# Kernel tuning notes

Hardware: AMD Instinct MI355X
Metric: run time of the kernel (lower is better)

Reference implementation:

```python
import jax, jax.numpy as jnp
from jax import lax
import numpy as np

BATCH, SEQ, VOCAB, EMB, UNIT = 256, 512, 50000, 128, 512


def setup_inputs() -> dict:
    key = jax.random.key(0)
    ks = jax.random.split(key, 8)
    s = 0.05  # keep tanh out of saturation
    return {
        "tokens": jax.random.randint(ks[0], (BATCH, SEQ), 0, VOCAB, dtype=jnp.int32),
        "emb": jax.random.normal(ks[1], (VOCAB, EMB), jnp.float32) * s,
        "Wx0": jax.random.normal(ks[2], (EMB, UNIT), jnp.float32) * s,
        "Wh0": jax.random.normal(ks[3], (UNIT, UNIT), jnp.float32) * s,
        "b0": jnp.zeros((UNIT,), jnp.float32),
        "Wx1": jax.random.normal(ks[4], (UNIT, UNIT), jnp.float32) * s,
        "Wh1": jax.random.normal(ks[5], (UNIT, UNIT), jnp.float32) * s,
        "b1": jnp.zeros((UNIT,), jnp.float32),
        "fc_w": jax.random.normal(ks[6], (UNIT, 1), jnp.float32) * s,
        "fc_b": jnp.zeros((1,), jnp.float32),
    }


def reference(tokens, emb, Wx0, Wh0, b0, Wx1, Wh1, b1, fc_w, fc_b):
    # Embedding lookup: [B, T, E]
    x = emb[tokens]
    B = tokens.shape[0]
    U = Wh0.shape[0]

    def step(carry, xt):
        h0, h1, h2 = carry
        # SimpleRNNCell: h' = tanh(x @ Wx + h @ Wh + b); dropout inactive (training=None)
        h0n = jnp.tanh(xt @ Wx0 + h0 @ Wh0 + b0)
        # NOTE: original code reuses rnncell1 weights for both layer 1 and layer 2 (bug kept)
        h1n = jnp.tanh(h0n @ Wx1 + h1 @ Wh1 + b1)
        h2n = jnp.tanh(h1n @ Wx1 + h2 @ Wh1 + b1)
        return (h0n, h1n, h2n), None

    init = tuple(jnp.zeros((B, U), x.dtype) for _ in range(3))
    (h0, h1, h2), _ = lax.scan(step, init, jnp.swapaxes(x, 0, 1))  # scan over time [T, B, E]
    logits = h2 @ fc_w + fc_b  # [B, 1]
    return jax.nn.sigmoid(logits)
```

## Files before the change

### kernel.cpp

```cpp
#include <hip/hip_runtime.h>


#define BATCH 256
#define SEQ   512
#define EMBD  128
#define UNIT  512

typedef _Float16 half8 __attribute__((ext_vector_type(8)));
typedef _Float16 half4 __attribute__((ext_vector_type(4)));
typedef float    f32x4 __attribute__((ext_vector_type(4)));
typedef unsigned int uint4v __attribute__((ext_vector_type(4)));
typedef int      int4v __attribute__((ext_vector_type(4)));

#define FLAGS_BYTES 4096
#define HBUF_OFF    4096
#define HBUF_ELEMS  (3*8*4*32*512)
#define HBUF_BYTES  (HBUF_ELEMS*2)
#define PWX0_OFF    (HBUF_OFF + HBUF_BYTES)
#define PWH0_OFF    (PWX0_OFF + EMBD*UNIT*2)
#define PWX1_OFF    (PWH0_OFF + UNIT*UNIT*2)
#define PWH1_OFF    (PWX1_OFF + UNIT*UNIT*2)

__device__ __forceinline__ void sc_st_int(int* p, int v) {
    asm volatile("global_store_dword %0, %1, off sc0 sc1" :: "v"(p), "v"(v) : "memory");
}

__device__ __forceinline__ void sc_ld_q3(const int* p0, const int* p1, const int* p2,
                                         int4v& a, int4v& b, int4v& c) {
    asm volatile(
        "global_load_dwordx4 %0, %3, off sc0 sc1\n\t"
        "global_load_dwordx4 %1, %4, off sc0 sc1\n\t"
        "global_load_dwordx4 %2, %5, off sc0 sc1\n\t"
        "s_waitcnt vmcnt(0)"
        : "=&v"(a), "=&v"(b), "=&v"(c)
        : "v"(p0), "v"(p1), "v"(p2)
        : "memory");
}

__device__ __forceinline__ void sc_load14(
    const uint4v* a0, const uint4v* a1, const uint4v* a2,
    const uint4v* a3, const uint4v* a4, const uint4v* a5,
    const uint4v* b0, const uint4v* b1, const uint4v* b2, const uint4v* b3,
    const uint4v* b4, const uint4v* b5, const uint4v* b6, const uint4v* b7,
    uint4v& s0, uint4v& s1, uint4v& s2, uint4v& s3, uint4v& s4, uint4v& s5,
    uint4v& r0, uint4v& r1, uint4v& r2, uint4v& r3,
    uint4v& r4, uint4v& r5, uint4v& r6, uint4v& r7)
{
    asm volatile(
        "global_load_dwordx4 %0, %14, off sc0 sc1\n\t"
        "global_load_dwordx4 %1, %15, off sc0 sc1\n\t"
        "global_load_dwordx4 %2, %16, off sc0 sc1\n\t"
        "global_load_dwordx4 %3, %17, off sc0 sc1\n\t"
        "global_load_dwordx4 %4, %18, off sc0 sc1\n\t"
        "global_load_dwordx4 %5, %19, off sc0 sc1\n\t"
        "global_load_dwordx4 %6, %20, off sc0 sc1\n\t"
        "global_load_dwordx4 %7, %21, off sc0 sc1\n\t"
        "global_load_dwordx4 %8, %22, off sc0 sc1\n\t"
        "global_load_dwordx4 %9, %23, off sc0 sc1\n\t"
        "global_load_dwordx4 %10, %24, off sc0 sc1\n\t"
        "global_load_dwordx4 %11, %25, off sc0 sc1\n\t"
        "global_load_dwordx4 %12, %26, off sc0 sc1\n\t"
        "global_load_dwordx4 %13, %27, off sc0 sc1\n\t"
        "s_waitcnt vmcnt(0)"
        : "=&v"(s0), "=&v"(s1), "=&v"(s2), "=&v"(s3), "=&v"(s4), "=&v"(s5),
          "=&v"(r0), "=&v"(r1), "=&v"(r2), "=&v"(r3),
          "=&v"(r4), "=&v"(r5), "=&v"(r6), "=&v"(r7)
        : "v"(a0), "v"(a1), "v"(a2), "v"(a3), "v"(a4), "v"(a5),
          "v"(b0), "v"(b1), "v"(b2), "v"(b3), "v"(b4), "v"(b5), "v"(b6), "v"(b7)
        : "memory");
}

__device__ __forceinline__ void sc_load6(
    const uint4v* p0, const uint4v* p1, const uint4v* p2,
    const uint4v* p3, const uint4v* p4, const uint4v* p5,
    uint4v& r0, uint4v& r1, uint4v& r2, uint4v& r3, uint4v& r4, uint4v& r5)
{
    asm volatile(
        "global_load_dwordx4 %0, %6, off sc0 sc1\n\t"
        "global_load_dwordx4 %1, %7, off sc0 sc1\n\t"
        "global_load_dwordx4 %2, %8, off sc0 sc1\n\t"
        "global_load_dwordx4 %3, %9, off sc0 sc1\n\t"
        "global_load_dwordx4 %4, %10, off sc0 sc1\n\t"
        "global_load_dwordx4 %5, %11, off sc0 sc1\n\t"
        "s_waitcnt vmcnt(0)"
        : "=&v"(r0), "=&v"(r1), "=&v"(r2), "=&v"(r3), "=&v"(r4), "=&v"(r5)
        : "v"(p0), "v"(p1), "v"(p2), "v"(p3), "v"(p4), "v"(p5)
        : "memory");
}

__device__ __forceinline__ void sc_store2(uint4v* p0, uint4v v0, uint4v* p1, uint4v v1) {
    asm volatile(
        "global_store_dwordx4 %0, %2, off sc0 sc1\n\t"
        "global_store_dwordx4 %1, %3, off sc0 sc1\n\t"
        "s_waitcnt vmcnt(0)"
        :: "v"(p0), "v"(p1), "v"(v0), "v"(v1)
        : "memory");
}

__global__ void zero_ws_kernel(uint4v* __restrict__ p, int n16) {
    int i = blockIdx.x * 256 + threadIdx.x;
    uint4v z = {0u, 0u, 0u, 0u};
    if (i < n16) p[i] = z;
}

__global__ void pack_w_kernel(const float* __restrict__ src, _Float16* __restrict__ dst,
                              int K, int N) {
    int idx = blockIdx.x * 256 + threadIdx.x;
    if (idx >= K * N) return;
    int j    = idx & 7;
    int lane = (idx >> 3) & 63;
    int rest = idx >> 9;
    int KT   = K >> 5;
    int kt   = rest % KT;
    int nt   = rest / KT;
    int k = kt*32 + (lane >> 4)*8 + j;
    int n = nt*16 + (lane & 15);
    dst[idx] = (_Float16)src[k * N + n];
}

__global__ __launch_bounds__(256, 1)
void rnn_main_kernel(const int*   __restrict__ tokens,
                     const float* __restrict__ emb,
                     const float* __restrict__ b0,
                     const float* __restrict__ b1,
                     char* ws)
{
    const int bid   = blockIdx.x;
    const int layer = bid >> 5;
    const int mg    = (bid >> 2) & 7;
    const int ns    = bid & 3;
    const int tid   = threadIdx.x;
    const int wv    = tid >> 6;
    const int lane  = tid & 63;
    const int q     = lane >> 4;
    const int c16   = lane & 15;

    int* flags = (int*)ws;
    int* qOwn  = flags + (layer*8 + mg)*32;
    int* qUp   = flags + ((layer > 0 ? layer-1 : layer)*8 + mg)*32;
    int* qDn   = flags + ((layer < 2 ? layer+1 : layer)*8 + mg)*32;

    _Float16* hbuf = (_Float16*)(ws + HBUF_OFF);
    const _Float16* pWh = (const _Float16*)(ws + (layer == 0 ? PWH0_OFF : PWH1_OFF));
    const _Float16* pWx = (const _Float16*)(ws + (layer == 0 ? PWX0_OFF : PWX1_OFF));
    const float* bias = (layer == 0) ? b0 : b1;

    const int c0  = ns*128 + wv*32;
    const int nt0 = c0 >> 4;

    __shared__ _Float16 Ah [32][512];
    __shared__ _Float16 Ain[32][512];
    __shared__ _Float16 Bounce[32][128];

    {
        uint4v z = {0u,0u,0u,0u};
#pragma unroll
        for (int i = 0; i < 8; ++i) ((uint4v*)Ah)[i*256 + tid] = z;
    }

    half8 whf[16][2];
    half8 wxf[16][2];
#pragma unroll
    for (int kt = 0; kt < 16; ++kt)
#pragma unroll
        for (int n = 0; n < 2; ++n)
            whf[kt][n] = *(const half8*)&pWh[(((nt0 + n)*16 + kt)*64 + lane) * 8];
    if (layer == 0) {
#pragma unroll
        for (int kt = 0; kt < 4; ++kt)
#pragma unroll
            for (int n = 0; n < 2; ++n)
                wxf[kt][n] = *(const half8*)&pWx[(((nt0 + n)*4 + kt)*64 + lane) * 8];
    } else {
#pragma unroll
        for (int kt = 0; kt < 16; ++kt)
#pragma unroll
            for (int n = 0; n < 2; ++n)
                wxf[kt][n] = *(const half8*)&pWx[(((nt0 + n)*16 + kt)*64 + lane) * 8];
    }

    const float bv0 = bias[c0 + c16];
    const float bv1 = bias[c0 + 16 + c16];

    const int m0       = mg * 32;
    const int slotBase = (layer*8 + mg) * 4;

    const int sA = (ns == 0) ? 1 : 0;
    const int sB = (ns <= 1) ? 2 : 1;
    const int sC = (ns <= 2) ? 3 : 2;

    for (int t = 0; t < SEQ; ++t) {
        if (tid == 0) {
            for (;;) {
                int4v o, u, d;
                sc_ld_q3(qOwn, qUp, qDn, o, u, d);
                int mo = o[0] < o[1] ? o[0] : o[1];
                mo = mo < o[2] ? mo : o[2]; mo = mo < o[3] ? mo : o[3];
                int mu = u[0] < u[1] ? u[0] : u[1];
                mu = mu < u[2] ? mu : u[2]; mu = mu < u[3] ? mu : u[3];
                int md = d[0] < d[1] ? d[0] : d[1];
                md = md < d[2] ? md : d[2]; md = md < d[3] ? md : d[3];
                bool ok = (mo >= t);
                if (layer > 0)            ok = ok && (mu >= t + 1);
                if (layer < 2 && t >= 4)  ok = ok && (md >= t - 3);
                if (ok) break;
                __builtin_amdgcn_s_sleep(1);
            }
        }
        __syncthreads();

        const uint4v* tp = (const uint4v*)(hbuf + (slotBase + ((t + 3) & 3)) * 16384);
        const int j0 = 2*tid, j1 = j0 + 1;
        const int r0i = j0 >> 4, cl0 = j0 & 15;
        const int r1i = j1 >> 4, cl1 = j1 & 15;
        const int ccA0 = sA*16 + cl0, ccA1 = sA*16 + cl1;
        const int ccB0 = sB*16 + cl0, ccB1 = sB*16 + cl1;
        const int ccC0 = sC*16 + cl0, ccC1 = sC*16 + cl1;

        f32x4 acc00 = {0,0,0,0}, acc01 = {0,0,0,0}, acc10 = {0,0,0,0}, acc11 = {0,0,0,0};

        if (layer > 0) {
            const uint4v* sb = (const uint4v*)
                (hbuf + (((layer-1)*8 + mg)*4 + (t & 3)) * 16384);
            uint4v s0,s1,s2,s3,s4,s5, rr0,rr1,rr2,rr3,rr4,rr5,rr6,rr7;
            sc_load14(tp + r0i*64 + ccA0, tp + r1i*64 + ccA1,
                      tp + r0i*64 + ccB0, tp + r1i*64 + ccB1,
                      tp + r0i*64 + ccC0, tp + r1i*64 + ccC1,
                      sb +        tid, sb +  256 + tid, sb +  512 + tid, sb +  768 + tid,
                      sb + 1024 + tid, sb + 1280 + tid, sb + 1536 + tid, sb + 1792 + tid,
                      s0, s1, s2, s3, s4, s5,
                      rr0, rr1, rr2, rr3, rr4, rr5, rr6, rr7);
            *(uint4v*)&Ah[r0i][((ccA0 + r0i) & 63) * 8] = s0;
            *(uint4v*)&Ah[r1i][((ccA1 + r1i) & 63) * 8] = s1;
            *(uint4v*)&Ah[r0i][((ccB0 + r0i) & 63) * 8] = s2;
            *(uint4v*)&Ah[r1i][((ccB1 + r1i) & 63) * 8] = s3;
            *(uint4v*)&Ah[r0i][((ccC0 + r0i) & 63) * 8] = s4;
            *(uint4v*)&Ah[r1i][((ccC1 + r1i) & 63) * 8] = s5;
#pragma unroll
            for (int i = 0; i < 8; ++i) {
                uint4v v = (i==0)?rr0:(i==1)?rr1:(i==2)?rr2:(i==3)?rr3:
                           (i==4)?rr4:(i==5)?rr5:(i==6)?rr6:rr7;
                int ci = i*256 + tid;
                int r  = ci >> 6;
                int cc = ci & 63;
                *(uint4v*)&Ain[r][((cc + r) & 63) * 8] = v;
            }
            __syncthreads();

#pragma unroll
            for (int kt = 0; kt < 16; ++kt) {
                half8 a0 = *(const half8*)&Ah[c16]     [((kt*4 + q + c16)      & 63) * 8];
                half8 a1 = *(const half8*)&Ah[16 + c16][((kt*4 + q + 16 + c16) & 63) * 8];
                acc00 = __builtin_amdgcn_mfma_f32_16x16x32_f16(a0, whf[kt][0], acc00, 0, 0, 0);
                acc01 = __builtin_amdgcn_mfma_f32_16x16x32_f16(a0, whf[kt][1], acc01, 0, 0, 0);
                acc10 = __builtin_amdgcn_mfma_f32_16x16x32_f16(a1, whf[kt][0], acc10, 0, 0, 0);
                acc11 = __builtin_amdgcn_mfma_f32_16x16x32_f16(a1, whf[kt][1], acc11, 0, 0, 0);
            }
#pragma unroll
            for (int kt = 0; kt < 16; ++kt) {
                half8 a0 = *(const half8*)&Ain[c16]     [((kt*4 + q + c16)      & 63) * 8];
                half8 a1 = *(const half8*)&Ain[16 + c16][((kt*4 + q + 16 + c16) & 63) * 8];
                acc00 = __builtin_amdgcn_mfma_f32_16x16x32_f16(a0, wxf[kt][0], acc00, 0, 0, 0);
                acc01 = __builtin_amdgcn_mfma_f32_16x16x32_f16(a0, wxf[kt][1], acc01, 0, 0, 0);
                acc10 = __builtin_amdgcn_mfma_f32_16x16x32_f16(a1, wxf[kt][0], acc10, 0, 0, 0);
                acc11 = __builtin_amdgcn_mfma_f32_16x16x32_f16(a1, wxf[kt][1], acc11, 0, 0, 0);
            }
        } else {
            uint4v s0, s1, s2, s3, s4, s5;
            sc_load6(tp + r0i*64 + ccA0, tp + r1i*64 + ccA1,
                     tp + r0i*64 + ccB0, tp + r1i*64 + ccB1,
                     tp + r0i*64 + ccC0, tp + r1i*64 + ccC1,
                     s0, s1, s2, s3, s4, s5);
            *(uint4v*)&Ah[r0i][((ccA0 + r0i) & 63) * 8] = s0;
            *(uint4v*)&Ah[r1i][((ccA1 + r1i) & 63) * 8] = s1;
            *(uint4v*)&Ah[r0i][((ccB0 + r0i) & 63) * 8] = s2;
            *(uint4v*)&Ah[r1i][((ccB1 + r1i) & 63) * 8] = s3;
            *(uint4v*)&Ah[r0i][((ccC0 + r0i) & 63) * 8] = s4;
            *(uint4v*)&Ah[r1i][((ccC1 + r1i) & 63) * 8] = s5;
#pragma unroll
            for (int i = 0; i < 4; ++i) {
                int idx = i*256 + tid;
                int r   = idx >> 5;
                int qq  = idx & 31;
                int tok = tokens[(m0 + r)*SEQ + t];
                float4 f = *((const float4*)(emb + (long)tok * EMBD) + qq);
                half4 h = { (_Float16)f.x, (_Float16)f.y, (_Float16)f.z, (_Float16)f.w };
                *(half4*)&Ain[r][((((qq >> 1) + r) & 63) * 8) + (qq & 1) * 4] = h;
            }
            __syncthreads();

#pragma unroll
            for (int kt = 0; kt < 16; ++kt) {
                half8 a0 = *(const half8*)&Ah[c16]     [((kt*4 + q + c16)      & 63) * 8];
                half8 a1 = *(const half8*)&Ah[16 + c16][((kt*4 + q + 16 + c16) & 63) * 8];
                acc00 = __builtin_amdgcn_mfma_f32_16x16x32_f16(a0, whf[kt][0], acc00, 0, 0, 0);
                acc01 = __builtin_amdgcn_mfma_f32_16x16x32_f16(a0, whf[kt][1], acc01, 0, 0, 0);
                acc10 = __builtin_amdgcn_mfma_f32_16x16x32_f16(a1, whf[kt][0], acc10, 0, 0, 0);
                acc11 = __builtin_amdgcn_mfma_f32_16x16x32_f16(a1, whf[kt][1], acc11, 0, 0, 0);
            }
#pragma unroll
            for (int kt = 0; kt < 4; ++kt) {
                half8 a0 = *(const half8*)&Ain[c16]     [((kt*4 + q + c16)      & 63) * 8];
                half8 a1 = *(const half8*)&Ain[16 + c16][((kt*4 + q + 16 + c16) & 63) * 8];
                acc00 = __builtin_amdgcn_mfma_f32_16x16x32_f16(a0, wxf[kt][0], acc00, 0, 0, 0);
                acc01 = __builtin_amdgcn_mfma_f32_16x16x32_f16(a0, wxf[kt][1], acc01, 0, 0, 0);
                acc10 = __builtin_amdgcn_mfma_f32_16x16x32_f16(a1, wxf[kt][0], acc10, 0, 0, 0);
                acc11 = __builtin_amdgcn_mfma_f32_16x16x32_f16(a1, wxf[kt][1], acc11, 0, 0, 0);
            }
        }

        _Float16 hv[16];
#pragma unroll
        for (int r = 0; r < 4; ++r) {
            int row0 = q*4 + r, row1 = 16 + row0;
            float z, e; _Float16 v;
            z = acc00[r] + bv0; e = __expf(2.0f*z); v = (_Float16)(1.0f - 2.0f/(e + 1.0f));
            hv[r*4+0] = v; Bounce[row0][wv*32 + c16]      = v;
            z = acc01[r] + bv1; e = __expf(2.0f*z); v = (_Float16)(1.0f - 2.0f/(e + 1.0f));
            hv[r*4+1] = v; Bounce[row0][wv*32 + 16 + c16] = v;
            z = acc10[r] + bv0; e = __expf(2.0f*z); v = (_Float16)(1.0f - 2.0f/(e + 1.0f));
            hv[r*4+2] = v; Bounce[row1][wv*32 + c16]      = v;
            z = acc11[r] + bv1; e = __expf(2.0f*z); v = (_Float16)(1.0f - 2.0f/(e + 1.0f));
            hv[r*4+3] = v; Bounce[row1][wv*32 + 16 + c16] = v;
        }
        __syncthreads();

        {
            int g0 = c0 + c16, g1 = c0 + 16 + c16;
#pragma unroll
            for (int r = 0; r < 4; ++r) {
                int row0 = q*4 + r, row1 = 16 + row0;
                Ah[row0][(((g0 >> 3) + row0) & 63)*8 + (g0 & 7)] = hv[r*4+0];
                Ah[row0][(((g1 >> 3) + row0) & 63)*8 + (g1 & 7)] = hv[r*4+1];
                Ah[row1][(((g0 >> 3) + row1) & 63)*8 + (g0 & 7)] = hv[r*4+2];
                Ah[row1][(((g1 >> 3) + row1) & 63)*8 + (g1 & 7)] = hv[r*4+3];
            }
            _Float16* tc = hbuf + (slotBase + (t & 3)) * 16384;
            uint4v v0 = ((const uint4v*)Bounce)[j0];
            uint4v v1 = ((const uint4v*)Bounce)[j1];
            uint4v* d0 = (uint4v*)(tc + (j0 >> 4)*512 + ns*128) + (j0 & 15);
            uint4v* d1 = (uint4v*)(tc + (j1 >> 4)*512 + ns*128) + (j1 & 15);
            sc_store2(d0, v0, d1, v1);
        }
        __syncthreads();
        if (tid == 0) sc_st_int(qOwn + ns, t + 1);
    }
}

__global__ void fc_kernel(const char* __restrict__ ws,
                          const float* __restrict__ fc_w,
                          const float* __restrict__ fc_b,
                          float* __restrict__ out)
{
    int row  = blockIdx.x;
    int lane = threadIdx.x;
    int m = row >> 5, lr = row & 31;
    const _Float16* h2 = (const _Float16*)(ws + HBUF_OFF)
                         + (((2*8 + m)*4 + 3) * 16384)
                         + lr * UNIT;
    half8 hv = *(const half8*)&h2[lane * 8];
    const float* w = fc_w + lane * 8;
    float s = 0.0f;
#pragma unroll
    for (int j = 0; j < 8; ++j) s += (float)hv[j] * w[j];
#pragma unroll
    for (int off = 32; off > 0; off >>= 1) s += __shfl_down(s, off);
    if (lane == 0) {
        float logit = s + fc_b[0];
        out[row] = 1.0f / (1.0f + __expf(-logit));
    }
}

extern "C" void kernel_launch(void* const* d_in, const int* in_sizes, int n_in,
                              void* d_out, int out_size, void* d_ws, size_t ws_size,
                              hipStream_t stream)
{
    const int*   tokens = (const int*)  d_in[0];
    const float* emb    = (const float*)d_in[1];
    const float* Wx0    = (const float*)d_in[2];
    const float* Wh0    = (const float*)d_in[3];
    const float* b0     = (const float*)d_in[4];
    const float* Wx1    = (const float*)d_in[5];
    const float* Wh1    = (const float*)d_in[6];
    const float* b1     = (const float*)d_in[7];
    const float* fcw    = (const float*)d_in[8];
    const float* fcb    = (const float*)d_in[9];
    char*  ws  = (char*)d_ws;
    float* out = (float*)d_out;

    int n16 = (FLAGS_BYTES + HBUF_BYTES) / 16;
    zero_ws_kernel<<<(n16 + 255)/256, 256, 0, stream>>>((uint4v*)ws, n16);

    pack_w_kernel<<<(EMBD*UNIT + 255)/256, 256, 0, stream>>>(Wx0, (_Float16*)(ws + PWX0_OFF), EMBD, UNIT);
    pack_w_kernel<<<(UNIT*UNIT + 255)/256, 256, 0, stream>>>(Wh0, (_Float16*)(ws + PWH0_OFF), UNIT, UNIT);
    pack_w_kernel<<<(UNIT*UNIT + 255)/256, 256, 0, stream>>>(Wx1, (_Float16*)(ws + PWX1_OFF), UNIT, UNIT);
    pack_w_kernel<<<(UNIT*UNIT + 255)/256, 256, 0, stream>>>(Wh1, (_Float16*)(ws + PWH1_OFF), UNIT, UNIT);

    rnn_main_kernel<<<96, 256, 0, stream>>>(tokens, emb, b0, b1, ws);

    fc_kernel<<<256, 64, 0, stream>>>((const char*)ws, fcw, fcb, out);
}
```

Before: 2.636 ms.

## Replace flag polling with per-element timestep tags in exchanged hidden states

Each fp16 hidden value is now stored as a 32-bit word whose upper 16 bits carry the timestep, so consumers detect readiness directly from the data. This drops the per-step producer flag polling, the barrier before loading, and the store wait. Loads for the next step are issued right after the current step's stores, so fetching overlaps with the next iteration's setup, and readers retry the whole load until every tag matches. Only a backpressure counter toward the downstream layer remains. In exchange the traffic doubles because of the tag words, and readers may retry repeatedly under contention.

```diff
diff --git a/kernel.cpp b/kernel.cpp
--- a/kernel.cpp
+++ b/kernel.cpp
@@ -10,12 +10,12 @@
 typedef _Float16 half4 __attribute__((ext_vector_type(4)));
 typedef float    f32x4 __attribute__((ext_vector_type(4)));
 typedef unsigned int uint4v __attribute__((ext_vector_type(4)));
-typedef int      int4v __attribute__((ext_vector_type(4)));
+typedef unsigned int uint2v __attribute__((ext_vector_type(2)));
 
 #define FLAGS_BYTES 4096
 #define HBUF_OFF    4096
-#define HBUF_ELEMS  (3*8*4*32*512)
-#define HBUF_BYTES  (HBUF_ELEMS*2)
+#define SLOT_BYTES  65536
+#define HBUF_BYTES  (3*8*4*SLOT_BYTES)
 #define PWX0_OFF    (HBUF_OFF + HBUF_BYTES)
 #define PWH0_OFF    (PWX0_OFF + EMBD*UNIT*2)
 #define PWX1_OFF    (PWH0_OFF + UNIT*UNIT*2)
@@ -24,82 +24,13 @@
 __device__ __forceinline__ void sc_st_int(int* p, int v) {
     asm volatile("global_store_dword %0, %1, off sc0 sc1" :: "v"(p), "v"(v) : "memory");
 }
-
-__device__ __forceinline__ void sc_ld_q3(const int* p0, const int* p1, const int* p2,
-                                         int4v& a, int4v& b, int4v& c) {
-    asm volatile(
-        "global_load_dwordx4 %0, %3, off sc0 sc1\n\t"
-        "global_load_dwordx4 %1, %4, off sc0 sc1\n\t"
-        "global_load_dwordx4 %2, %5, off sc0 sc1\n\t"
-        "s_waitcnt vmcnt(0)"
-        : "=&v"(a), "=&v"(b), "=&v"(c)
-        : "v"(p0), "v"(p1), "v"(p2)
-        : "memory");
-}
-
-__device__ __forceinline__ void sc_load14(
-    const uint4v* a0, const uint4v* a1, const uint4v* a2,
-    const uint4v* a3, const uint4v* a4, const uint4v* a5,
-    const uint4v* b0, const uint4v* b1, const uint4v* b2, const uint4v* b3,
-    const uint4v* b4, const uint4v* b5, const uint4v* b6, const uint4v* b7,
-    uint4v& s0, uint4v& s1, uint4v& s2, uint4v& s3, uint4v& s4, uint4v& s5,
-    uint4v& r0, uint4v& r1, uint4v& r2, uint4v& r3,
-    uint4v& r4, uint4v& r5, uint4v& r6, uint4v& r7)
-{
-    asm volatile(
-        "global_load_dwordx4 %0, %14, off sc0 sc1\n\t"
-        "global_load_dwordx4 %1, %15, off sc0 sc1\n\t"
-        "global_load_dwordx4 %2, %16, off sc0 sc1\n\t"
-        "global_load_dwordx4 %3, %17, off sc0 sc1\n\t"
-        "global_load_dwordx4 %4, %18, off sc0 sc1\n\t"
-        "global_load_dwordx4 %5, %19, off sc0 sc1\n\t"
-        "global_load_dwordx4 %6, %20, off sc0 sc1\n\t"
-        "global_load_dwordx4 %7, %21, off sc0 sc1\n\t"
-        "global_load_dwordx4 %8, %22, off sc0 sc1\n\t"
-        "global_load_dwordx4 %9, %23, off sc0 sc1\n\t"
-        "global_load_dwordx4 %10, %24, off sc0 sc1\n\t"
-        "global_load_dwordx4 %11, %25, off sc0 sc1\n\t"
-        "global_load_dwordx4 %12, %26, off sc0 sc1\n\t"
-        "global_load_dwordx4 %13, %27, off sc0 sc1\n\t"
-        "s_waitcnt vmcnt(0)"
-        : "=&v"(s0), "=&v"(s1), "=&v"(s2), "=&v"(s3), "=&v"(s4), "=&v"(s5),
-          "=&v"(r0), "=&v"(r1), "=&v"(r2), "=&v"(r3),
-          "=&v"(r4), "=&v"(r5), "=&v"(r6), "=&v"(r7)
-        : "v"(a0), "v"(a1), "v"(a2), "v"(a3), "v"(a4), "v"(a5),
-          "v"(b0), "v"(b1), "v"(b2), "v"(b3), "v"(b4), "v"(b5), "v"(b6), "v"(b7)
-        : "memory");
-}
-
-__device__ __forceinline__ void sc_load6(
-    const uint4v* p0, const uint4v* p1, const uint4v* p2,
-    const uint4v* p3, const uint4v* p4, const uint4v* p5,
-    uint4v& r0, uint4v& r1, uint4v& r2, uint4v& r3, uint4v& r4, uint4v& r5)
-{
-    asm volatile(
-        "global_load_dwordx4 %0, %6, off sc0 sc1\n\t"
-        "global_load_dwordx4 %1, %7, off sc0 sc1\n\t"
-        "global_load_dwordx4 %2, %8, off sc0 sc1\n\t"
-        "global_load_dwordx4 %3, %9, off sc0 sc1\n\t"
-        "global_load_dwordx4 %4, %10, off sc0 sc1\n\t"
-        "global_load_dwordx4 %5, %11, off sc0 sc1\n\t"
-        "s_waitcnt vmcnt(0)"
-        : "=&v"(r0), "=&v"(r1), "=&v"(r2), "=&v"(r3), "=&v"(r4), "=&v"(r5)
-        : "v"(p0), "v"(p1), "v"(p2), "v"(p3), "v"(p4), "v"(p5)
-        : "memory");
-}
-
-__device__ __forceinline__ void sc_store2(uint4v* p0, uint4v v0, uint4v* p1, uint4v v1) {
-    asm volatile(
-        "global_store_dwordx4 %0, %2, off sc0 sc1\n\t"
-        "global_store_dwordx4 %1, %3, off sc0 sc1\n\t"
-        "s_waitcnt vmcnt(0)"
-        :: "v"(p0), "v"(p1), "v"(v0), "v"(v1)
-        : "memory");
-}
-
-__global__ void zero_ws_kernel(uint4v* __restrict__ p, int n16) {
+__device__ __forceinline__ unsigned hbits(_Float16 h) {
+    union { _Float16 f; unsigned short u; } x; x.f = h; return (unsigned)x.u;
+}
+
+__global__ void fill_ws_kernel(uint4v* __restrict__ p, int n16, unsigned pat) {
     int i = blockIdx.x * 256 + threadIdx.x;
-    uint4v z = {0u, 0u, 0u, 0u};
+    uint4v z = {pat, pat, pat, pat};
     if (i < n16) p[i] = z;
 }
 
@@ -117,6 +48,25 @@
     int n = nt*16 + (lane & 15);
     dst[idx] = (_Float16)src[k * N + n];
 }
+
+#define STAGE_SIB(Q, CS, II) do {                                              \
+    int r_   = (II)*8 + (tid >> 5);                                            \
+    int ch0_ = (CS) + (tid & 31)*4;                                            \
+    unsigned lo_ = ((Q)[0] & 0xFFFFu) | ((Q)[1] << 16);                        \
+    unsigned hi_ = ((Q)[2] & 0xFFFFu) | ((Q)[3] << 16);                        \
+    *(uint2v*)((unsigned*)&Ah[r_][0] +                                         \
+        ((((ch0_ >> 3) + r_) & 63)*4 + ((ch0_ >> 2) & 1)*2)) = (uint2v){lo_, hi_}; \
+} while (0)
+
+#define STAGE_AIN(Q, II) do {                                                  \
+    int m_  = (II)*256 + tid;                                                  \
+    int r_  = m_ >> 7;                                                         \
+    int cg_ = m_ & 127;                                                        \
+    unsigned lo_ = ((Q)[0] & 0xFFFFu) | ((Q)[1] << 16);                        \
+    unsigned hi_ = ((Q)[2] & 0xFFFFu) | ((Q)[3] << 16);                        \
+    *(uint2v*)((unsigned*)&Ain[r_][0] +                                        \
+        ((((cg_ >> 1) + r_) & 63)*4 + (cg_ & 1)*2)) = (uint2v){lo_, hi_};      \
+} while (0)
 
 __global__ __launch_bounds__(256, 1)
 void rnn_main_kernel(const int*   __restrict__ tokens,
@@ -135,22 +85,29 @@
     const int q     = lane >> 4;
     const int c16   = lane & 15;
 
-    int* flags = (int*)ws;
-    int* qOwn  = flags + (layer*8 + mg)*32;
-    int* qUp   = flags + ((layer > 0 ? layer-1 : layer)*8 + mg)*32;
-    int* qDn   = flags + ((layer < 2 ? layer+1 : layer)*8 + mg)*32;
-
-    _Float16* hbuf = (_Float16*)(ws + HBUF_OFF);
+    int* flags  = (int*)ws;
+    int* qDn    = flags + ((layer < 2 ? layer + 1 : layer)*8 + mg)*32;
+    int* myCons = flags + (layer*8 + mg)*32 + ns;
+
+    char* hbuf = ws + HBUF_OFF;
     const _Float16* pWh = (const _Float16*)(ws + (layer == 0 ? PWH0_OFF : PWH1_OFF));
     const _Float16* pWx = (const _Float16*)(ws + (layer == 0 ? PWX0_OFF : PWX1_OFF));
     const float* bias = (layer == 0) ? b0 : b1;
 
     const int c0  = ns*128 + wv*32;
     const int nt0 = c0 >> 4;
-
-    __shared__ _Float16 Ah [32][512];
-    __shared__ _Float16 Ain[32][512];
-    __shared__ _Float16 Bounce[32][128];
+    const int m0  = mg * 32;
+    const int bc0 = ns * 128;
+
+    const int sA = (ns == 0) ? 1 : 0;
+    const int sB = (ns <= 1) ? 2 : 1;
+    const int sC = (ns <= 2) ? 3 : 2;
+    const int CsA = sA*128, CsB = sB*128, CsC = sC*128;
+
+    __shared__ __align__(16) _Float16 Ah [32][512];
+    __shared__ __align__(16) _Float16 Ain[32][512];
+    __shared__ __align__(16) unsigned Bounce[32][128];
+    __shared__ int wflag[4];
 
     {
         uint4v z = {0u,0u,0u,0u};
@@ -182,101 +139,140 @@
     const float bv0 = bias[c0 + c16];
     const float bv1 = bias[c0 + 16 + c16];
 
-    const int m0       = mg * 32;
-    const int slotBase = (layer*8 + mg) * 4;
-
-    const int sA = (ns == 0) ? 1 : 0;
-    const int sB = (ns <= 1) ? 2 : 1;
-    const int sC = (ns <= 2) ? 3 : 2;
+    const unsigned voff_sib = ((unsigned)(tid >> 5))*2048u + ((unsigned)(tid & 31))*16u;
+    const unsigned vsf0 = voff_sib, vsf1 = voff_sib + 16384u,
+                   vsf2 = voff_sib + 32768u, vsf3 = voff_sib + 49152u;
+    const unsigned vaf0 = (unsigned)tid*16u, vaf1 = vaf0 + 4096u,
+                   vaf2 = vaf0 + 8192u, vaf3 = vaf0 + 12288u;
+    const unsigned voff_st = ((unsigned)(tid >> 3))*2048u + ((unsigned)(tid & 7))*64u;
+
+    uint4v s0,s1,s2,s3,s4,s5,s6,s7,s8,s9,s10,s11;
+    uint4v a0,a1,a2,a3,a4,a5,a6,a7,a8,a9,a10,a11,a12,a13,a14,a15;
+    uint4v fq;
+    uint4v sv0 = {0,0,0,0}, sv1 = {0,0,0,0}, sv2 = {0,0,0,0}, sv3 = {0,0,0,0};
+
+    auto issue_all = [&](int tt) {
+        {
+            const char* sb = hbuf + (size_t)((layer*8 + mg)*4 + ((tt + 3) & 3)) * SLOT_BYTES;
+            const char* bA = sb + CsA*4;
+            const char* bB = sb + CsB*4;
+            const char* bC = sb + CsC*4;
+            asm volatile(
+                "global_load_dwordx4 %0,  %12, %16 sc0 sc1\n\t"
+                "global_load_dwordx4 %1,  %13, %16 sc0 sc1\n\t"
+                "global_load_dwordx4 %2,  %14, %16 sc0 sc1\n\t"
+                "global_load_dwordx4 %3,  %15, %16 sc0 sc1\n\t"
+                "global_load_dwordx4 %4,  %12, %17 sc0 sc1\n\t"
+                "global_load_dwordx4 %5,  %13, %17 sc0 sc1\n\t"
+                "global_load_dwordx4 %6,  %14, %17 sc0 sc1\n\t"
+                "global_load_dwordx4 %7,  %15, %17 sc0 sc1\n\t"
+                "global_load_dwordx4 %8,  %12, %18 sc0 sc1\n\t"
+                "global_load_dwordx4 %9,  %13, %18 sc0 sc1\n\t"
+                "global_load_dwordx4 %10, %14, %18 sc0 sc1\n\t"
+                "global_load_dwordx4 %11, %15, %18 sc0 sc1"
+                : "=&v"(s0),"=&v"(s1),"=&v"(s2),"=&v"(s3),"=&v"(s4),"=&v"(s5),
+                  "=&v"(s6),"=&v"(s7),"=&v"(s8),"=&v"(s9),"=&v"(s10),"=&v"(s11)
+                : "v"(vsf0),"v"(vsf1),"v"(vsf2),"v"(vsf3),"s"(bA),"s"(bB),"s"(bC)
+                : "memory");
+            asm volatile("global_load_dwordx4 %0, %1, off sc0 sc1"
+                : "=&v"(fq) : "v"(qDn) : "memory");
+        }
+        if (layer > 0) {
+            const char* ab = hbuf + (size_t)(((layer - 1)*8 + mg)*4 + (tt & 3)) * SLOT_BYTES;
+            asm volatile(
+                "global_load_dwordx4 %0, %8,  %12 sc0 sc1\n\t"
+                "global_load_dwordx4 %1, %9,  %12 sc0 sc1\n\t"
+                "global_load_dwordx4 %2, %10, %12 sc0 sc1\n\t"
+                "global_load_dwordx4 %3, %11, %12 sc0 sc1\n\t"
+                "global_load_dwordx4 %4, %8,  %13 sc0 sc1\n\t"
+                "global_load_dwordx4 %5, %9,  %13 sc0 sc1\n\t"
+                "global_load_dwordx4 %6, %10, %13 sc0 sc1\n\t"
+                "global_load_dwordx4 %7, %11, %13 sc0 sc1"
+                : "=&v"(a0),"=&v"(a1),"=&v"(a2),"=&v"(a3),
+                  "=&v"(a4),"=&v"(a5),"=&v"(a6),"=&v"(a7)
+                : "v"(vaf0),"v"(vaf1),"v"(vaf2),"v"(vaf3),"s"(ab),"s"(ab + 16384)
+                : "memory");
+            asm volatile(
+                "global_load_dwordx4 %0, %8,  %12 sc0 sc1\n\t"
+                "global_load_dwordx4 %1, %9,  %12 sc0 sc1\n\t"
+                "global_load_dwordx4 %2, %10, %12 sc0 sc1\n\t"
+                "global_load_dwordx4 %3, %11, %12 sc0 sc1\n\t"
+                "global_load_dwordx4 %4, %8,  %13 sc0 sc1\n\t"
+                "global_load_dwordx4 %5, %9,  %13 sc0 sc1\n\t"
+                "global_load_dwordx4 %6, %10, %13 sc0 sc1\n\t"
+                "global_load_dwordx4 %7, %11, %13 sc0 sc1"
+                : "=&v"(a8),"=&v"(a9),"=&v"(a10),"=&v"(a11),
+                  "=&v"(a12),"=&v"(a13),"=&v"(a14),"=&v"(a15)
+                : "v"(vaf0),"v"(vaf1),"v"(vaf2),"v"(vaf3),"s"(ab + 32768),"s"(ab + 49152)
+                : "memory");
+        }
+    };
+
+    issue_all(0);
 
     for (int t = 0; t < SEQ; ++t) {
-        if (tid == 0) {
-            for (;;) {
-                int4v o, u, d;
-                sc_ld_q3(qOwn, qUp, qDn, o, u, d);
-                int mo = o[0] < o[1] ? o[0] : o[1];
-                mo = mo < o[2] ? mo : o[2]; mo = mo < o[3] ? mo : o[3];
-                int mu = u[0] < u[1] ? u[0] : u[1];
-                mu = mu < u[2] ? mu : u[2]; mu = mu < u[3] ? mu : u[3];
-                int md = d[0] < d[1] ? d[0] : d[1];
-                md = md < d[2] ? md : d[2]; md = md < d[3] ? md : d[3];
-                bool ok = (mo >= t);
-                if (layer > 0)            ok = ok && (mu >= t + 1);
-                if (layer < 2 && t >= 4)  ok = ok && (md >= t - 3);
-                if (ok) break;
-                __builtin_amdgcn_s_sleep(1);
-            }
-        }
-        __syncthreads();
-
-        const uint4v* tp = (const uint4v*)(hbuf + (slotBase + ((t + 3) & 3)) * 16384);
-        const int j0 = 2*tid, j1 = j0 + 1;
-        const int r0i = j0 >> 4, cl0 = j0 & 15;
-        const int r1i = j1 >> 4, cl1 = j1 & 15;
-        const int ccA0 = sA*16 + cl0, ccA1 = sA*16 + cl1;
-        const int ccB0 = sB*16 + cl0, ccB1 = sB*16 + cl1;
-        const int ccC0 = sC*16 + cl0, ccC1 = sC*16 + cl1;
-
-        f32x4 acc00 = {0,0,0,0}, acc01 = {0,0,0,0}, acc10 = {0,0,0,0}, acc11 = {0,0,0,0};
+        const unsigned exps = ((unsigned)((t - 1) & 0xFFFF)) << 16;
+        const unsigned expa = ((unsigned)( t      & 0xFFFF)) << 16;
+        const uint4v exps4 = {exps, exps, exps, exps};
+        const uint4v expa4 = {expa, expa, expa, expa};
+
+        for (;;) {
+            asm volatile("s_waitcnt vmcnt(0)"
+                : "+v"(s0),"+v"(s1),"+v"(s2),"+v"(s3),"+v"(s4),"+v"(s5),
+                  "+v"(s6),"+v"(s7),"+v"(s8),"+v"(s9),"+v"(s10),"+v"(s11)
+                : "v"(sv0),"v"(sv1),"v"(sv2),"v"(sv3)
+                : "memory");
+            if (layer > 0) {
+                asm volatile("" : "+v"(a0),"+v"(a1),"+v"(a2),"+v"(a3),
+                                  "+v"(a4),"+v"(a5),"+v"(a6),"+v"(a7) :: "memory");
+                asm volatile("" : "+v"(a8),"+v"(a9),"+v"(a10),"+v"(a11),
+                                  "+v"(a12),"+v"(a13),"+v"(a14),"+v"(a15),"+v"(fq) :: "memory");
+            } else {
+                asm volatile("" : "+v"(fq) :: "memory");
+            }
+
+            uint4v badv = {0u,0u,0u,0u};
+            badv |= (s0 ^ exps4);  badv |= (s1 ^ exps4);  badv |= (s2  ^ exps4);
+            badv |= (s3 ^ exps4);  badv |= (s4 ^ exps4);  badv |= (s5  ^ exps4);
+            badv |= (s6 ^ exps4);  badv |= (s7 ^ exps4);  badv |= (s8  ^ exps4);
+            badv |= (s9 ^ exps4);  badv |= (s10 ^ exps4); badv |= (s11 ^ exps4);
+            if (layer > 0) {
+                badv |= (a0  ^ expa4); badv |= (a1  ^ expa4); badv |= (a2  ^ expa4);
+                badv |= (a3  ^ expa4); badv |= (a4  ^ expa4); badv |= (a5  ^ expa4);
+                badv |= (a6  ^ expa4); badv |= (a7  ^ expa4); badv |= (a8  ^ expa4);
+                badv |= (a9  ^ expa4); badv |= (a10 ^ expa4); badv |= (a11 ^ expa4);
+                badv |= (a12 ^ expa4); badv |= (a13 ^ expa4); badv |= (a14 ^ expa4);
+                badv |= (a15 ^ expa4);
+            }
+            unsigned bad = (badv[0] | badv[1] | badv[2] | badv[3]) & 0xFFFF0000u;
+            if (layer < 2) {
+                int mn = (int)fq[0];
+                mn = ((int)fq[1] < mn) ? (int)fq[1] : mn;
+                mn = ((int)fq[2] < mn) ? (int)fq[2] : mn;
+                mn = ((int)fq[3] < mn) ? (int)fq[3] : mn;
+                if (mn < t - 3) bad |= 1u;
+            }
+            unsigned long long wb = __ballot(bad != 0u);
+            if (lane == 0) wflag[wv] = (wb != 0ull) ? 1 : 0;
+            __syncthreads();
+            int any = wflag[0] | wflag[1] | wflag[2] | wflag[3];
+            __syncthreads();
+            if (!any) break;
+            issue_all(t);
+        }
+
+        if (layer > 0 && tid == 0) sc_st_int(myCons, t + 1);
+
+        STAGE_SIB(s0, CsA, 0); STAGE_SIB(s1, CsA, 1); STAGE_SIB(s2,  CsA, 2); STAGE_SIB(s3,  CsA, 3);
+        STAGE_SIB(s4, CsB, 0); STAGE_SIB(s5, CsB, 1); STAGE_SIB(s6,  CsB, 2); STAGE_SIB(s7,  CsB, 3);
+        STAGE_SIB(s8, CsC, 0); STAGE_SIB(s9, CsC, 1); STAGE_SIB(s10, CsC, 2); STAGE_SIB(s11, CsC, 3);
 
         if (layer > 0) {
-            const uint4v* sb = (const uint4v*)
-                (hbuf + (((layer-1)*8 + mg)*4 + (t & 3)) * 16384);
-            uint4v s0,s1,s2,s3,s4,s5, rr0,rr1,rr2,rr3,rr4,rr5,rr6,rr7;
-            sc_load14(tp + r0i*64 + ccA0, tp + r1i*64 + ccA1,
-                      tp + r0i*64 + ccB0, tp + r1i*64 + ccB1,
-                      tp + r0i*64 + ccC0, tp + r1i*64 + ccC1,
-                      sb +        tid, sb +  256 + tid, sb +  512 + tid, sb +  768 + tid,
-                      sb + 1024 + tid, sb + 1280 + tid, sb + 1536 + tid, sb + 1792 + tid,
-                      s0, s1, s2, s3, s4, s5,
-                      rr0, rr1, rr2, rr3, rr4, rr5, rr6, rr7);
-            *(uint4v*)&Ah[r0i][((ccA0 + r0i) & 63) * 8] = s0;
-            *(uint4v*)&Ah[r1i][((ccA1 + r1i) & 63) * 8] = s1;
-            *(uint4v*)&Ah[r0i][((ccB0 + r0i) & 63) * 8] = s2;
-            *(uint4v*)&Ah[r1i][((ccB1 + r1i) & 63) * 8] = s3;
-            *(uint4v*)&Ah[r0i][((ccC0 + r0i) & 63) * 8] = s4;
-            *(uint4v*)&Ah[r1i][((ccC1 + r1i) & 63) * 8] = s5;
-#pragma unroll
-            for (int i = 0; i < 8; ++i) {
-                uint4v v = (i==0)?rr0:(i==1)?rr1:(i==2)?rr2:(i==3)?rr3:
-                           (i==4)?rr4:(i==5)?rr5:(i==6)?rr6:rr7;
-                int ci = i*256 + tid;
-                int r  = ci >> 6;
-                int cc = ci & 63;
-                *(uint4v*)&Ain[r][((cc + r) & 63) * 8] = v;
-            }
-            __syncthreads();
-
-#pragma unroll
-            for (int kt = 0; kt < 16; ++kt) {
-                half8 a0 = *(const half8*)&Ah[c16]     [((kt*4 + q + c16)      & 63) * 8];
-                half8 a1 = *(const half8*)&Ah[16 + c16][((kt*4 + q + 16 + c16) & 63) * 8];
-                acc00 = __builtin_amdgcn_mfma_f32_16x16x32_f16(a0, whf[kt][0], acc00, 0, 0, 0);
-                acc01 = __builtin_amdgcn_mfma_f32_16x16x32_f16(a0, whf[kt][1], acc01, 0, 0, 0);
-                acc10 = __builtin_amdgcn_mfma_f32_16x16x32_f16(a1, whf[kt][0], acc10, 0, 0, 0);
-                acc11 = __builtin_amdgcn_mfma_f32_16x16x32_f16(a1, whf[kt][1], acc11, 0, 0, 0);
-            }
-#pragma unroll
-            for (int kt = 0; kt < 16; ++kt) {
-                half8 a0 = *(const half8*)&Ain[c16]     [((kt*4 + q + c16)      & 63) * 8];
-                half8 a1 = *(const half8*)&Ain[16 + c16][((kt*4 + q + 16 + c16) & 63) * 8];
-                acc00 = __builtin_amdgcn_mfma_f32_16x16x32_f16(a0, wxf[kt][0], acc00, 0, 0, 0);
-                acc01 = __builtin_amdgcn_mfma_f32_16x16x32_f16(a0, wxf[kt][1], acc01, 0, 0, 0);
-                acc10 = __builtin_amdgcn_mfma_f32_16x16x32_f16(a1, wxf[kt][0], acc10, 0, 0, 0);
-                acc11 = __builtin_amdgcn_mfma_f32_16x16x32_f16(a1, wxf[kt][1], acc11, 0, 0, 0);
-            }
+            STAGE_AIN(a0, 0);  STAGE_AIN(a1, 1);  STAGE_AIN(a2, 2);  STAGE_AIN(a3, 3);
+            STAGE_AIN(a4, 4);  STAGE_AIN(a5, 5);  STAGE_AIN(a6, 6);  STAGE_AIN(a7, 7);
+            STAGE_AIN(a8, 8);  STAGE_AIN(a9, 9);  STAGE_AIN(a10,10); STAGE_AIN(a11,11);
+            STAGE_AIN(a12,12); STAGE_AIN(a13,13); STAGE_AIN(a14,14); STAGE_AIN(a15,15);
         } else {
-            uint4v s0, s1, s2, s3, s4, s5;
-            sc_load6(tp + r0i*64 + ccA0, tp + r1i*64 + ccA1,
-                     tp + r0i*64 + ccB0, tp + r1i*64 + ccB1,
-                     tp + r0i*64 + ccC0, tp + r1i*64 + ccC1,
-                     s0, s1, s2, s3, s4, s5);
-            *(uint4v*)&Ah[r0i][((ccA0 + r0i) & 63) * 8] = s0;
-            *(uint4v*)&Ah[r1i][((ccA1 + r1i) & 63) * 8] = s1;
-            *(uint4v*)&Ah[r0i][((ccB0 + r0i) & 63) * 8] = s2;
-            *(uint4v*)&Ah[r1i][((ccB1 + r1i) & 63) * 8] = s3;
-            *(uint4v*)&Ah[r0i][((ccC0 + r0i) & 63) * 8] = s4;
-            *(uint4v*)&Ah[r1i][((ccC1 + r1i) & 63) * 8] = s5;
 #pragma unroll
             for (int i = 0; i < 4; ++i) {
                 int idx = i*256 + tid;
@@ -287,41 +283,65 @@
                 half4 h = { (_Float16)f.x, (_Float16)f.y, (_Float16)f.z, (_Float16)f.w };
                 *(half4*)&Ain[r][((((qq >> 1) + r) & 63) * 8) + (qq & 1) * 4] = h;
             }
-            __syncthreads();
-
+        }
+        __syncthreads();
+
+        f32x4 acc00 = {0,0,0,0}, acc01 = {0,0,0,0}, acc10 = {0,0,0,0}, acc11 = {0,0,0,0};
+
+        if (layer > 0) {
 #pragma unroll
             for (int kt = 0; kt < 16; ++kt) {
-                half8 a0 = *(const half8*)&Ah[c16]     [((kt*4 + q + c16)      & 63) * 8];
-                half8 a1 = *(const half8*)&Ah[16 + c16][((kt*4 + q + 16 + c16) & 63) * 8];
-                acc00 = __builtin_amdgcn_mfma_f32_16x16x32_f16(a0, whf[kt][0], acc00, 0, 0, 0);
-                acc01 = __builtin_amdgcn_mfma_f32_16x16x32_f16(a0, whf[kt][1], acc01, 0, 0, 0);
-                acc10 = __builtin_amdgcn_mfma_f32_16x16x32_f16(a1, whf[kt][0], acc10, 0, 0, 0);
-                acc11 = __builtin_amdgcn_mfma_f32_16x16x32_f16(a1, whf[kt][1], acc11, 0, 0, 0);
+                half8 fa0 = *(const half8*)&Ah[c16]     [((kt*4 + q + c16)      & 63) * 8];
+                half8 fa1 = *(const half8*)&Ah[16 + c16][((kt*4 + q + 16 + c16) & 63) * 8];
+                acc00 = __builtin_amdgcn_mfma_f32_16x16x32_f16(fa0, whf[kt][0], acc00, 0, 0, 0);
+                acc01 = __builtin_amdgcn_mfma_f32_16x16x32_f16(fa0, whf[kt][1], acc01, 0, 0, 0);
+                acc10 = __builtin_amdgcn_mfma_f32_16x16x32_f16(fa1, whf[kt][0], acc10, 0, 0, 0);
+                acc11 = __builtin_amdgcn_mfma_f32_16x16x32_f16(fa1, whf[kt][1], acc11, 0, 0, 0);
+            }
+#pragma unroll
+            for (int kt = 0; kt < 16; ++kt) {
+                half8 fa0 = *(const half8*)&Ain[c16]     [((kt*4 + q + c16)      & 63) * 8];
+                half8 fa1 = *(const half8*)&Ain[16 + c16][((kt*4 + q + 16 + c16) & 63) * 8];
+                acc00 = __builtin_amdgcn_mfma_f32_16x16x32_f16(fa0, wxf[kt][0], acc00, 0, 0, 0);
+                acc01 = __builtin_amdgcn_mfma_f32_16x16x32_f16(fa0, wxf[kt][1], acc01, 0, 0, 0);
+                acc10 = __builtin_amdgcn_mfma_f32_16x16x32_f16(fa1, wxf[kt][0], acc10, 0, 0, 0);
+                acc11 = __builtin_amdgcn_mfma_f32_16x16x32_f16(fa1, wxf[kt][1], acc11, 0, 0, 0);
+            }
+        } else {
+#pragma unroll
+            for (int kt = 0; kt < 16; ++kt) {
+                half8 fa0 = *(const half8*)&Ah[c16]     [((kt*4 + q + c16)      & 63) * 8];
+                half8 fa1 = *(const half8*)&Ah[16 + c16][((kt*4 + q + 16 + c16) & 63) * 8];
+                acc00 = __builtin_amdgcn_mfma_f32_16x16x32_f16(fa0, whf[kt][0], acc00, 0, 0, 0);
+                acc01 = __builtin_amdgcn_mfma_f32_16x16x32_f16(fa0, whf[kt][1], acc01, 0, 0, 0);
+                acc10 = __builtin_amdgcn_mfma_f32_16x16x32_f16(fa1, whf[kt][0], acc10, 0, 0, 0);
+                acc11 = __builtin_amdgcn_mfma_f32_16x16x32_f16(fa1, whf[kt][1], acc11, 0, 0, 0);
             }
 #pragma unroll
             for (int kt = 0; kt < 4; ++kt) {
-                half8 a0 = *(const half8*)&Ain[c16]     [((kt*4 + q + c16)      & 63) * 8];
-                half8 a1 = *(const half8*)&Ain[16 + c16][((kt*4 + q + 16 + c16) & 63) * 8];
-                acc00 = __builtin_amdgcn_mfma_f32_16x16x32_f16(a0, wxf[kt][0], acc00, 0, 0, 0);
-                acc01 = __builtin_amdgcn_mfma_f32_16x16x32_f16(a0, wxf[kt][1], acc01, 0, 0, 0);
-                acc10 = __builtin_amdgcn_mfma_f32_16x16x32_f16(a1, wxf[kt][0], acc10, 0, 0, 0);
-                acc11 = __builtin_amdgcn_mfma_f32_16x16x32_f16(a1, wxf[kt][1], acc11, 0, 0, 0);
-            }
-        }
-
+                half8 fa0 = *(const half8*)&Ain[c16]     [((kt*4 + q + c16)      & 63) * 8];
+                half8 fa1 = *(const half8*)&Ain[16 + c16][((kt*4 + q + 16 + c16) & 63) * 8];
+                acc00 = __builtin_amdgcn_mfma_f32_16x16x32_f16(fa0, wxf[kt][0], acc00, 0, 0, 0);
+                acc01 = __builtin_amdgcn_mfma_f32_16x16x32_f16(fa0, wxf[kt][1], acc01, 0, 0, 0);
+                acc10 = __builtin_amdgcn_mfma_f32_16x16x32_f16(fa1, wxf[kt][0], acc10, 0, 0, 0);
+                acc11 = __builtin_amdgcn_mfma_f32_16x16x32_f16(fa1, wxf[kt][1], acc11, 0, 0, 0);
+            }
+        }
+
+        const unsigned tagw = ((unsigned)t) << 16;
         _Float16 hv[16];
 #pragma unroll
         for (int r = 0; r < 4; ++r) {
             int row0 = q*4 + r, row1 = 16 + row0;
             float z, e; _Float16 v;
             z = acc00[r] + bv0; e = __expf(2.0f*z); v = (_Float16)(1.0f - 2.0f/(e + 1.0f));
-            hv[r*4+0] = v; Bounce[row0][wv*32 + c16]      = v;
+            hv[r*4+0] = v; Bounce[row0][wv*32 + c16]      = tagw | hbits(v);
             z = acc01[r] + bv1; e = __expf(2.0f*z); v = (_Float16)(1.0f - 2.0f/(e + 1.0f));
-            hv[r*4+1] = v; Bounce[row0][wv*32 + 16 + c16] = v;
+            hv[r*4+1] = v; Bounce[row0][wv*32 + 16 + c16] = tagw | hbits(v);
             z = acc10[r] + bv0; e = __expf(2.0f*z); v = (_Float16)(1.0f - 2.0f/(e + 1.0f));
-            hv[r*4+2] = v; Bounce[row1][wv*32 + c16]      = v;
+            hv[r*4+2] = v; Bounce[row1][wv*32 + c16]      = tagw | hbits(v);
             z = acc11[r] + bv1; e = __expf(2.0f*z); v = (_Float16)(1.0f - 2.0f/(e + 1.0f));
-            hv[r*4+3] = v; Bounce[row1][wv*32 + 16 + c16] = v;
+            hv[r*4+3] = v; Bounce[row1][wv*32 + 16 + c16] = tagw | hbits(v);
         }
         __syncthreads();
 
@@ -335,16 +355,26 @@
                 Ah[row1][(((g0 >> 3) + row1) & 63)*8 + (g0 & 7)] = hv[r*4+2];
                 Ah[row1][(((g1 >> 3) + row1) & 63)*8 + (g1 & 7)] = hv[r*4+3];
             }
-            _Float16* tc = hbuf + (slotBase + (t & 3)) * 16384;
-            uint4v v0 = ((const uint4v*)Bounce)[j0];
-            uint4v v1 = ((const uint4v*)Bounce)[j1];
-            uint4v* d0 = (uint4v*)(tc + (j0 >> 4)*512 + ns*128) + (j0 & 15);
-            uint4v* d1 = (uint4v*)(tc + (j1 >> 4)*512 + ns*128) + (j1 & 15);
-            sc_store2(d0, v0, d1, v1);
-        }
-        __syncthreads();
-        if (tid == 0) sc_st_int(qOwn + ns, t + 1);
+        }
+
+        {
+            const uint4v* bp = (const uint4v*)&Bounce[0][0];
+            sv0 = bp[4*tid + 0]; sv1 = bp[4*tid + 1];
+            sv2 = bp[4*tid + 2]; sv3 = bp[4*tid + 3];
+            const char* stb = hbuf + (size_t)((layer*8 + mg)*4 + (t & 3)) * SLOT_BYTES + bc0*4;
+            asm volatile(
+                "global_store_dwordx4 %4, %0, %5 sc0 sc1\n\t"
+                "global_store_dwordx4 %4, %1, %5 offset:16 sc0 sc1\n\t"
+                "global_store_dwordx4 %4, %2, %5 offset:32 sc0 sc1\n\t"
+                "global_store_dwordx4 %4, %3, %5 offset:48 sc0 sc1"
+                :: "v"(sv0),"v"(sv1),"v"(sv2),"v"(sv3),"v"(voff_st),"s"(stb)
+                : "memory");
+        }
+
+        if (t + 1 < SEQ) issue_all(t + 1);
     }
+
+    asm volatile("s_waitcnt vmcnt(0)" :: "v"(sv0),"v"(sv1),"v"(sv2),"v"(sv3) : "memory");
 }
 
 __global__ void fc_kernel(const char* __restrict__ ws,
@@ -355,14 +385,16 @@
     int row  = blockIdx.x;
     int lane = threadIdx.x;
     int m = row >> 5, lr = row & 31;
-    const _Float16* h2 = (const _Float16*)(ws + HBUF_OFF)
-                         + (((2*8 + m)*4 + 3) * 16384)
+    const unsigned* h2 = (const unsigned*)(ws + HBUF_OFF
+                         + (size_t)(((2*8 + m)*4 + 3)) * SLOT_BYTES)
                          + lr * UNIT;
-    half8 hv = *(const half8*)&h2[lane * 8];
-    const float* w = fc_w + lane * 8;
     float s = 0.0f;
 #pragma unroll
-    for (int j = 0; j < 8; ++j) s += (float)hv[j] * w[j];
+    for (int j = 0; j < 8; ++j) {
+        unsigned d = h2[lane*8 + j];
+        union { unsigned short u; _Float16 f; } x; x.u = (unsigned short)(d & 0xFFFFu);
+        s += (float)x.f * fc_w[lane*8 + j];
+    }
 #pragma unroll
     for (int off = 32; off > 0; off >>= 1) s += __shfl_down(s, off);
     if (lane == 0) {
@@ -388,8 +420,10 @@
     char*  ws  = (char*)d_ws;
     float* out = (float*)d_out;
 
-    int n16 = (FLAGS_BYTES + HBUF_BYTES) / 16;
-    zero_ws_kernel<<<(n16 + 255)/256, 256, 0, stream>>>((uint4v*)ws, n16);
+    int n16f = FLAGS_BYTES / 16;
+    fill_ws_kernel<<<(n16f + 255)/256, 256, 0, stream>>>((uint4v*)ws, n16f, 0u);
+    int n16r = HBUF_BYTES / 16;
+    fill_ws_kernel<<<(n16r + 255)/256, 256, 0, stream>>>((uint4v*)(ws + HBUF_OFF), n16r, 0xFFFF0000u);
 
     pack_w_kernel<<<(EMBD*UNIT + 255)/256, 256, 0, stream>>>(Wx0, (_Float16*)(ws + PWX0_OFF), EMBD, UNIT);
     pack_w_kernel<<<(UNIT*UNIT + 255)/256, 256, 0, stream>>>(Wh0, (_Float16*)(ws + PWH0_OFF), UNIT, UNIT);
```

Result: slower. 5.339 ms (+102.6%).
